# Optimization experiments

Measured on AMD Instinct MI355X. Metric: run time of the kernel, lower is better.

## Reference

```python
import jax, jax.numpy as jnp
import numpy as np

N_VOLS, N_PARTS = 4, 8          # hard-coded in GL.forward
B = N_VOLS * N_PARTS            # asserted batch size = 32
DIM, HID, PROJ = 8192, 4096, 256
TEMP = 0.1
BN_EPS = 1e-5


def setup_inputs() -> dict:
    key = jax.random.key(0)
    k = jax.random.split(key, 5)
    s1 = 1.0 / np.sqrt(DIM)
    s2 = 1.0 / np.sqrt(HID)
    return {
        "x": jax.random.normal(k[0], (B, DIM), jnp.float32),
        "W1": jax.random.uniform(k[1], (DIM, HID), jnp.float32, -s1, s1),
        "b1": jax.random.uniform(k[2], (HID,), jnp.float32, -s1, s1),
        "gamma": jnp.ones((HID,), jnp.float32),
        "beta": jnp.zeros((HID,), jnp.float32),
        "W2": jax.random.uniform(k[3], (HID, PROJ), jnp.float32, -s2, s2),
        "b2": jax.random.uniform(k[4], (PROJ,), jnp.float32, -s2, s2),
    }


def _gl_loss(proj):
    # F.normalize(p=2, dim=-1); CosineSimilarity on unit vectors == dot product
    p = proj / jnp.linalg.norm(proj, axis=-1, keepdims=True)
    sims = (p @ p.T) / TEMP                       # [B, B]
    idx = jnp.arange(B)
    # pos_index(i) = {i % n_parts + v * n_parts} -> same part id; includes i itself
    pos_mask = (idx[:, None] % N_PARTS) == (idx[None, :] % N_PARTS)  # [B, B], 4 per row
    neg_mask = ~pos_mask                                             # 28 per row
    E = jnp.exp(sims)                              # original uses raw exp (no max-shift)
    row_neg = jnp.sum(jnp.where(neg_mask, E, 0.0), axis=1)    # sum_j exp(s[i, neg_j])
    ET = E.T                                        # ET[i, p] = exp(s[p, i])
    col_neg = jnp.sum(jnp.where(neg_mask, ET, 0.0), axis=1)   # sum_j exp(s[neg_j, i])
    t1 = -jnp.log(E / (E + row_neg[:, None]))      # row-direction term per (i, pos)
    t2 = -jnp.log(ET / (ET + col_neg[:, None]))    # column-direction term per (i, pos)
    per_row = jnp.sum(jnp.where(pos_mask, t1 + t2, 0.0), axis=1) / N_VOLS
    return jnp.sum(per_row) / (B * 2)


def reference(x, W1, b1, gamma, beta, W2, b2):
    # projector MLP: Linear -> BatchNorm1d (training stats) -> ReLU -> Linear
    h = x @ W1 + b1
    mu = jnp.mean(h, axis=0)
    var = jnp.var(h, axis=0)                       # biased variance, BN training mode
    h = gamma * (h - mu) * jax.lax.rsqrt(var + BN_EPS) + beta
    h = jax.nn.relu(h)
    proj = h @ W2 + b2                             # [B, PROJ]
    return _gl_loss(proj)
```

## Files before the change

kernel.cpp:

```cpp
#include <hip/hip_runtime.h>

#define DIM   8192
#define HID   4096
#define PROJ  256
#define NB    32
#define KSP1  16
#define KCH1  (DIM / KSP1)
#define KT1   (KCH1 / 32)
#define KSP2  16
#define KCH2  (HID / KSP2)
#define KT2   (KCH2 / 32)

typedef __attribute__((ext_vector_type(8))) short bf16x8;
typedef __attribute__((ext_vector_type(4))) float f32x4;

__device__ __forceinline__ float bf2f(unsigned short u) {
    return __uint_as_float(((unsigned)u) << 16);
}
__device__ __forceinline__ unsigned short f2bf(float f) {
    unsigned u = __float_as_uint(f);
    u += 0x7fffu + ((u >> 16) & 1u);
    return (unsigned short)(u >> 16);
}
__device__ __forceinline__ unsigned pk2(float a, float b) {
    return (unsigned)f2bf(a) | ((unsigned)f2bf(b) << 16);
}

__device__ __forceinline__ bool detect_bf16(const unsigned* __restrict__ xw, int lane) {
    unsigned v = xw[lane];
    int e = (int)((v >> 7) & 0xffu);
    bool pl = (e >= 100 && e <= 135);
    unsigned long long b = __ballot(pl);
    return __popcll(b) >= 32;
}

__global__ __launch_bounds__(256, 4) void gemm1_kernel(
    const void* __restrict__ xv, const void* __restrict__ W1v,
    float* __restrict__ hpart)
{
    const int t  = threadIdx.x;
    const int nb = blockIdx.x & 63;
    const int kc = blockIdx.x >> 6;
    const int k0 = kc * KCH1;

    const bool isbf = detect_bf16((const unsigned*)xv, t & 63);
    const unsigned short* xu  = (const unsigned short*)xv;
    const float*          xf  = (const float*)xv;
    const unsigned short* W1u = (const unsigned short*)W1v;
    const float*          W1f = (const float*)W1v;

    const int lane  = t & 63;
    const int w     = t >> 6;
    const int g     = lane >> 4;
    const int ln    = lane & 15;
    const int nbase = nb * 64 + w * 16;

    auto loadB = [&](int kt) -> bf16x8 {
        bf16x8 b;
        const long rb = (long)(k0 + kt * 32 + g * 8) * HID + nbase + ln;
        if (isbf) {
            #pragma unroll
            for (int j = 0; j < 8; ++j) b[j] = (short)W1u[rb + (long)j * HID];
        } else {
            #pragma unroll
            for (int j = 0; j < 8; ++j) b[j] = (short)f2bf(W1f[rb + (long)j * HID]);
        }
        return b;
    };
    auto loadA = [&](int kt, int mt) -> bf16x8 {
        const int base = (mt * 16 + ln) * DIM + k0 + kt * 32 + g * 8;
        if (isbf) return *(const bf16x8*)(xu + base);
        float4 f0 = *(const float4*)(xf + base);
        float4 f1 = *(const float4*)(xf + base + 4);
        union { uint4 u; bf16x8 v; } c;
        c.u = make_uint4(pk2(f0.x, f0.y), pk2(f0.z, f0.w),
                         pk2(f1.x, f1.y), pk2(f1.z, f1.w));
        return c.v;
    };

    bf16x8 bb[4], a0[4], a1[4];
    #pragma unroll
    for (int i = 0; i < 4; ++i) {
        bb[i] = loadB(i); a0[i] = loadA(i, 0); a1[i] = loadA(i, 1);
    }

    f32x4 acc0 = {0.f, 0.f, 0.f, 0.f};
    f32x4 acc1 = {0.f, 0.f, 0.f, 0.f};

    #pragma unroll
    for (int kt = 0; kt < KT1; ++kt) {
        const int s = kt & 3;
        acc0 = __builtin_amdgcn_mfma_f32_16x16x32_bf16(a0[s], bb[s], acc0, 0, 0, 0);
        acc1 = __builtin_amdgcn_mfma_f32_16x16x32_bf16(a1[s], bb[s], acc1, 0, 0, 0);
        if (kt + 4 < KT1) {
            bb[s] = loadB(kt + 4);
            a0[s] = loadA(kt + 4, 0);
            a1[s] = loadA(kt + 4, 1);
        }
    }

    const int col = nbase + ln;
    #pragma unroll
    for (int r = 0; r < 4; ++r) {
        hpart[(kc * NB + g * 4 + r) * HID + col]      = acc0[r];
        hpart[(kc * NB + 16 + g * 4 + r) * HID + col] = acc1[r];
    }
}

__global__ __launch_bounds__(256) void bnrelu_kernel(
    const float* __restrict__ hpart, const void* __restrict__ gv,
    const void* __restrict__ bev, unsigned short* __restrict__ hrelu,
    const void* __restrict__ xv)
{
    __shared__ float red[16][64];
    __shared__ float ssc[64], sbe[64], smu[64];
    const int t  = threadIdx.x;
    const int c4 = t & 15, q = t >> 4;
    const int n0 = blockIdx.x * 64;
    const int nb = n0 + c4 * 4;
    const bool isbf = detect_bf16((const unsigned*)xv, t & 63);

    f32x4 h0 = {0.f, 0.f, 0.f, 0.f};
    f32x4 h1 = {0.f, 0.f, 0.f, 0.f};
    #pragma unroll
    for (int kc = 0; kc < KSP1; ++kc) {
        h0 += *(const f32x4*)(hpart + (size_t)(kc * 32 + 2 * q) * HID + nb);
        h1 += *(const f32x4*)(hpart + (size_t)(kc * 32 + 2 * q + 1) * HID + nb);
    }
    *(f32x4*)&red[q][c4 * 4] = h0 + h1;
    __syncthreads();
    if (t < 64) {
        float s = 0.f;
        #pragma unroll
        for (int i = 0; i < 16; ++i) s += red[i][t];
        smu[t] = s * (1.f / 32.f);
    }
    __syncthreads();
    const f32x4 mu = *(const f32x4*)&smu[c4 * 4];
    const f32x4 d0 = h0 - mu, d1 = h1 - mu;
    *(f32x4*)&red[q][c4 * 4] = d0 * d0 + d1 * d1;
    __syncthreads();
    if (t < 64) {
        float v = 0.f;
        #pragma unroll
        for (int i = 0; i < 16; ++i) v += red[i][t];
        v *= (1.f / 32.f);
        const int nn = n0 + t;
        const float ga = isbf ? bf2f(((const unsigned short*)gv)[nn])  : ((const float*)gv)[nn];
        const float be = isbf ? bf2f(((const unsigned short*)bev)[nn]) : ((const float*)bev)[nn];
        ssc[t] = ga * rsqrtf(v + 1e-5f);
        sbe[t] = be;
    }
    __syncthreads();
    const f32x4 sc = *(const f32x4*)&ssc[c4 * 4];
    const f32x4 be = *(const f32x4*)&sbe[c4 * 4];
    f32x4 r0 = d0 * sc + be;
    f32x4 r1 = d1 * sc + be;
    ushort4 o0, o1;
    o0.x = f2bf(fmaxf(r0.x, 0.f)); o0.y = f2bf(fmaxf(r0.y, 0.f));
    o0.z = f2bf(fmaxf(r0.z, 0.f)); o0.w = f2bf(fmaxf(r0.w, 0.f));
    o1.x = f2bf(fmaxf(r1.x, 0.f)); o1.y = f2bf(fmaxf(r1.y, 0.f));
    o1.z = f2bf(fmaxf(r1.z, 0.f)); o1.w = f2bf(fmaxf(r1.w, 0.f));
    *(ushort4*)(hrelu + (size_t)(2 * q) * HID + nb)     = o0;
    *(ushort4*)(hrelu + (size_t)(2 * q + 1) * HID + nb) = o1;
}

__global__ __launch_bounds__(256, 4) void gemm2_kernel(
    const unsigned short* __restrict__ hrelu, const void* __restrict__ W2v,
    float* __restrict__ ppart, const void* __restrict__ xv)
{
    const int t  = threadIdx.x;
    const int nb = blockIdx.x & 3;
    const int kc = blockIdx.x >> 2;
    const int k0 = kc * KCH2;

    const bool isbf = detect_bf16((const unsigned*)xv, t & 63);
    const unsigned short* W2u = (const unsigned short*)W2v;
    const float*          W2f = (const float*)W2v;

    const int lane  = t & 63;
    const int w     = t >> 6;
    const int g     = lane >> 4;
    const int ln    = lane & 15;
    const int nbase = nb * 64 + w * 16;

    auto loadB = [&](int kt) -> bf16x8 {
        bf16x8 b;
        const long rb = (long)(k0 + kt * 32 + g * 8) * PROJ + nbase + ln;
        if (isbf) {
            #pragma unroll
            for (int j = 0; j < 8; ++j) b[j] = (short)W2u[rb + (long)j * PROJ];
        } else {
            #pragma unroll
            for (int j = 0; j < 8; ++j) b[j] = (short)f2bf(W2f[rb + (long)j * PROJ]);
        }
        return b;
    };
    auto loadA = [&](int kt, int mt) -> bf16x8 {
        return *(const bf16x8*)(hrelu + (mt * 16 + ln) * HID + k0 + kt * 32 + g * 8);
    };

    bf16x8 bb[4], a0[4], a1[4];
    #pragma unroll
    for (int i = 0; i < 4; ++i) {
        bb[i] = loadB(i); a0[i] = loadA(i, 0); a1[i] = loadA(i, 1);
    }

    f32x4 acc0 = {0.f, 0.f, 0.f, 0.f};
    f32x4 acc1 = {0.f, 0.f, 0.f, 0.f};

    #pragma unroll
    for (int kt = 0; kt < KT2; ++kt) {
        const int s = kt & 3;
        acc0 = __builtin_amdgcn_mfma_f32_16x16x32_bf16(a0[s], bb[s], acc0, 0, 0, 0);
        acc1 = __builtin_amdgcn_mfma_f32_16x16x32_bf16(a1[s], bb[s], acc1, 0, 0, 0);
        if (kt + 4 < KT2) {
            bb[s] = loadB(kt + 4);
            a0[s] = loadA(kt + 4, 0);
            a1[s] = loadA(kt + 4, 1);
        }
    }

    const int col = nbase + ln;
    #pragma unroll
    for (int r = 0; r < 4; ++r) {
        ppart[(kc * NB + g * 4 + r) * PROJ + col]      = acc0[r];
        ppart[(kc * NB + 16 + g * 4 + r) * PROJ + col] = acc1[r];
    }
}

__global__ __launch_bounds__(1024) void loss_kernel(
    const float* __restrict__ ppart, const void* __restrict__ b2v,
    const void* __restrict__ xv, unsigned* __restrict__ out)
{
    __shared__ float ps[32][260];
    __shared__ float npart2[32][8];
    __shared__ float inrm[32];
    __shared__ float rowtot[32];
    const int t = threadIdx.x;
    const bool isbf = detect_bf16((const unsigned*)xv, t & 63);

    #pragma unroll
    for (int i = 0; i < 8; ++i) {
        const int o = i * 1024 + t;
        float s = 0.f;
        #pragma unroll
        for (int s16 = 0; s16 < KSP2; ++s16) s += ppart[s16 * (NB * PROJ) + o];
        const int c = o & 255;
        s += isbf ? bf2f(((const unsigned short*)b2v)[c]) : ((const float*)b2v)[c];
        ps[o >> 8][c] = s;
    }
    __syncthreads();

    if (t < 256) {
        const int r = t >> 3, seg = t & 7;
        float s = 0.f;
        #pragma unroll
        for (int c = 0; c < 32; ++c) { float v = ps[r][seg * 32 + c]; s += v * v; }
        npart2[r][seg] = s;
    }
    __syncthreads();
    if (t < 32) {
        float s = 0.f;
        #pragma unroll
        for (int j = 0; j < 8; ++j) s += npart2[t][j];
        inrm[t] = rsqrtf(s);
    }
    __syncthreads();

    const int wv   = t >> 6;
    const int lane = t & 63;
    const int j    = (lane >> 1) & 31;
    const int half = lane & 1;
    #pragma unroll
    for (int rr = 0; rr < 2; ++rr) {
        const int i = wv * 2 + rr;
        float acc = 0.f;
        const int cb = half * 128;
        #pragma unroll
        for (int c = 0; c < 128; c += 4) {
            float4 a = *(const float4*)&ps[i][cb + c];
            float4 b = *(const float4*)&ps[j][cb + c];
            acc += a.x * b.x + a.y * b.y + a.z * b.z + a.w * b.w;
        }
        acc += __shfl_xor(acc, 1);

        const float sim = acc * inrm[i] * inrm[j] * 10.0f;
        const float E   = __expf(sim);
        const bool pos  = ((j & 7) == (i & 7));

        float nv = (!pos && half == 0) ? E : 0.f;
        #pragma unroll
        for (int s = 1; s < 64; s <<= 1) nv += __shfl_xor(nv, s);
        float pv = (pos && half == 0) ? (logf(E + nv) - sim) : 0.f;
        #pragma unroll
        for (int s = 1; s < 64; s <<= 1) pv += __shfl_xor(pv, s);
        if (lane == 0) rowtot[i] = pv;
    }
    __syncthreads();

    if (t < 64) {
        float v = (t < 32) ? rowtot[t] : 0.f;
        #pragma unroll
        for (int s = 1; s < 64; s <<= 1) v += __shfl_xor(v, s);
        if (t == 0) {
            const float loss = v * (1.0f / 128.0f);
            const unsigned lb = (unsigned)f2bf(loss);
            const unsigned base = (__float_as_uint(loss) & 0xffff0000u) | lb;
            unsigned best = base;
            float ebest = fabsf(__uint_as_float(base) - loss);
            const unsigned cp = base + 0x10000u;
            const float ep = fabsf(__uint_as_float(cp) - loss);
            if (ep < ebest) { best = cp; ebest = ep; }
            const unsigned cm = base - 0x10000u;
            const float em = fabsf(__uint_as_float(cm) - loss);
            if (em < ebest) { best = cm; }
            out[0] = best;
        }
    }
}

extern "C" void kernel_launch(void* const* d_in, const int* in_sizes, int n_in,
                              void* d_out, int out_size, void* d_ws, size_t ws_size,
                              hipStream_t stream) {
    const void* x  = d_in[0];
    const void* W1 = d_in[1];
    const void* ga = d_in[3];
    const void* be = d_in[4];
    const void* W2 = d_in[5];
    const void* b2 = d_in[6];

    char* wsp = (char*)d_ws;
    float* hpart = (float*)wsp;                 wsp += (size_t)KSP1 * NB * HID * 4;
    unsigned short* hrelu = (unsigned short*)wsp; wsp += (size_t)NB * HID * 2;
    float* ppart = (float*)wsp;                 wsp += (size_t)KSP2 * NB * PROJ * 4;

    gemm1_kernel<<<1024, 256, 0, stream>>>(x, W1, hpart);
    bnrelu_kernel<<<64, 256, 0, stream>>>(hpart, ga, be, hrelu, x);
    gemm2_kernel<<<64, 256, 0, stream>>>(hrelu, W2, ppart, x);
    loss_kernel<<<1, 1024, 0, stream>>>(ppart, b2, x, (unsigned*)d_out);
}
```

Baseline: 240.2 us.

## Cut GEMM prefetch depth to two stages and simplify address and pack arithmetic

In both GEMM kernels, the four-deep register prefetch ring is replaced by a two-stage double buffer with explicit A/B slots. Loads are now indexed with precomputed 32-bit base offsets instead of per-load 64-bit address math. The fp32-to-bf16 pack uses a single byte-permute builtin instead of shifts and ors. The aim is fewer VGPRs and less integer overhead, at the cost of fewer loads in flight to hide global-memory latency in a bandwidth-bound GEMM.

```diff
diff --git a/kernel.cpp b/kernel.cpp
--- a/kernel.cpp
+++ b/kernel.cpp
@@ -23,7 +23,11 @@
     return (unsigned short)(u >> 16);
 }
 __device__ __forceinline__ unsigned pk2(float a, float b) {
-    return (unsigned)f2bf(a) | ((unsigned)f2bf(b) << 16);
+    unsigned ua = __float_as_uint(a);
+    unsigned ub = __float_as_uint(b);
+    ua += 0x7fffu + ((ua >> 16) & 1u);
+    ub += 0x7fffu + ((ub >> 16) & 1u);
+    return __builtin_amdgcn_perm(ub, ua, 0x07060302u);
 }
 
 __device__ __forceinline__ bool detect_bf16(const unsigned* __restrict__ xw, int lane) {
@@ -55,20 +59,29 @@
     const int ln    = lane & 15;
     const int nbase = nb * 64 + w * 16;
 
+    const unsigned ubB = (unsigned)(k0 + g * 8) * HID + (unsigned)(nbase + ln);
+    const unsigned ubA0 = (unsigned)(0 * 16 + ln) * DIM + (unsigned)(k0 + g * 8);
+    const unsigned ubA1 = (unsigned)(1 * 16 + ln) * DIM + (unsigned)(k0 + g * 8);
+
     auto loadB = [&](int kt) -> bf16x8 {
-        bf16x8 b;
-        const long rb = (long)(k0 + kt * 32 + g * 8) * HID + nbase + ln;
+        union { unsigned u[4]; bf16x8 v; } r;
         if (isbf) {
             #pragma unroll
-            for (int j = 0; j < 8; ++j) b[j] = (short)W1u[rb + (long)j * HID];
+            for (int j = 0; j < 8; ++j)
+                ((unsigned short*)r.u)[j] = W1u[ubB + (unsigned)(kt * 32 + j) * HID];
         } else {
-            #pragma unroll
-            for (int j = 0; j < 8; ++j) b[j] = (short)f2bf(W1f[rb + (long)j * HID]);
-        }
-        return b;
+            float f[8];
+            #pragma unroll
+            for (int j = 0; j < 8; ++j)
+                f[j] = W1f[ubB + (unsigned)(kt * 32 + j) * HID];
+            #pragma unroll
+            for (int j = 0; j < 4; ++j)
+                r.u[j] = pk2(f[2 * j], f[2 * j + 1]);
+        }
+        return r.v;
     };
     auto loadA = [&](int kt, int mt) -> bf16x8 {
-        const int base = (mt * 16 + ln) * DIM + k0 + kt * 32 + g * 8;
+        const unsigned base = (mt ? ubA1 : ubA0) + (unsigned)(kt * 32);
         if (isbf) return *(const bf16x8*)(xu + base);
         float4 f0 = *(const float4*)(xf + base);
         float4 f1 = *(const float4*)(xf + base + 4);
@@ -78,24 +91,23 @@
         return c.v;
     };
 
-    bf16x8 bb[4], a0[4], a1[4];
-    #pragma unroll
-    for (int i = 0; i < 4; ++i) {
-        bb[i] = loadB(i); a0[i] = loadA(i, 0); a1[i] = loadA(i, 1);
-    }
+    bf16x8 bA  = loadB(0), aA0 = loadA(0, 0), aA1 = loadA(0, 1);
+    bf16x8 bB  = loadB(1), aB0 = loadA(1, 0), aB1 = loadA(1, 1);
 
     f32x4 acc0 = {0.f, 0.f, 0.f, 0.f};
     f32x4 acc1 = {0.f, 0.f, 0.f, 0.f};
 
     #pragma unroll
-    for (int kt = 0; kt < KT1; ++kt) {
-        const int s = kt & 3;
-        acc0 = __builtin_amdgcn_mfma_f32_16x16x32_bf16(a0[s], bb[s], acc0, 0, 0, 0);
-        acc1 = __builtin_amdgcn_mfma_f32_16x16x32_bf16(a1[s], bb[s], acc1, 0, 0, 0);
-        if (kt + 4 < KT1) {
-            bb[s] = loadB(kt + 4);
-            a0[s] = loadA(kt + 4, 0);
-            a1[s] = loadA(kt + 4, 1);
+    for (int kt = 0; kt < KT1; kt += 2) {
+        acc0 = __builtin_amdgcn_mfma_f32_16x16x32_bf16(aA0, bA, acc0, 0, 0, 0);
+        acc1 = __builtin_amdgcn_mfma_f32_16x16x32_bf16(aA1, bA, acc1, 0, 0, 0);
+        if (kt + 2 < KT1) {
+            bA = loadB(kt + 2); aA0 = loadA(kt + 2, 0); aA1 = loadA(kt + 2, 1);
+        }
+        acc0 = __builtin_amdgcn_mfma_f32_16x16x32_bf16(aB0, bB, acc0, 0, 0, 0);
+        acc1 = __builtin_amdgcn_mfma_f32_16x16x32_bf16(aB1, bB, acc1, 0, 0, 0);
+        if (kt + 3 < KT1) {
+            bB = loadB(kt + 3); aB0 = loadA(kt + 3, 0); aB1 = loadA(kt + 3, 1);
         }
     }
 
@@ -184,40 +196,48 @@
     const int ln    = lane & 15;
     const int nbase = nb * 64 + w * 16;
 
+    const unsigned ubB = (unsigned)(k0 + g * 8) * PROJ + (unsigned)(nbase + ln);
+    const unsigned ubA0 = (unsigned)(0 * 16 + ln) * HID + (unsigned)(k0 + g * 8);
+    const unsigned ubA1 = (unsigned)(1 * 16 + ln) * HID + (unsigned)(k0 + g * 8);
+
     auto loadB = [&](int kt) -> bf16x8 {
-        bf16x8 b;
-        const long rb = (long)(k0 + kt * 32 + g * 8) * PROJ + nbase + ln;
+        union { unsigned u[4]; bf16x8 v; } r;
         if (isbf) {
             #pragma unroll
-            for (int j = 0; j < 8; ++j) b[j] = (short)W2u[rb + (long)j * PROJ];
+            for (int j = 0; j < 8; ++j)
+                ((unsigned short*)r.u)[j] = W2u[ubB + (unsigned)(kt * 32 + j) * PROJ];
         } else {
-            #pragma unroll
-            for (int j = 0; j < 8; ++j) b[j] = (short)f2bf(W2f[rb + (long)j * PROJ]);
-        }
-        return b;
+            float f[8];
+            #pragma unroll
+            for (int j = 0; j < 8; ++j)
+                f[j] = W2f[ubB + (unsigned)(kt * 32 + j) * PROJ];
+            #pragma unroll
+            for (int j = 0; j < 4; ++j)
+                r.u[j] = pk2(f[2 * j], f[2 * j + 1]);
+        }
+        return r.v;
     };
     auto loadA = [&](int kt, int mt) -> bf16x8 {
-        return *(const bf16x8*)(hrelu + (mt * 16 + ln) * HID + k0 + kt * 32 + g * 8);
+        return *(const bf16x8*)(hrelu + (mt ? ubA1 : ubA0) + (unsigned)(kt * 32));
     };
 
-    bf16x8 bb[4], a0[4], a1[4];
-    #pragma unroll
-    for (int i = 0; i < 4; ++i) {
-        bb[i] = loadB(i); a0[i] = loadA(i, 0); a1[i] = loadA(i, 1);
-    }
+    bf16x8 bA  = loadB(0), aA0 = loadA(0, 0), aA1 = loadA(0, 1);
+    bf16x8 bB  = loadB(1), aB0 = loadA(1, 0), aB1 = loadA(1, 1);
 
     f32x4 acc0 = {0.f, 0.f, 0.f, 0.f};
     f32x4 acc1 = {0.f, 0.f, 0.f, 0.f};
 
     #pragma unroll
-    for (int kt = 0; kt < KT2; ++kt) {
-        const int s = kt & 3;
-        acc0 = __builtin_amdgcn_mfma_f32_16x16x32_bf16(a0[s], bb[s], acc0, 0, 0, 0);
-        acc1 = __builtin_amdgcn_mfma_f32_16x16x32_bf16(a1[s], bb[s], acc1, 0, 0, 0);
-        if (kt + 4 < KT2) {
-            bb[s] = loadB(kt + 4);
-            a0[s] = loadA(kt + 4, 0);
-            a1[s] = loadA(kt + 4, 1);
+    for (int kt = 0; kt < KT2; kt += 2) {
+        acc0 = __builtin_amdgcn_mfma_f32_16x16x32_bf16(aA0, bA, acc0, 0, 0, 0);
+        acc1 = __builtin_amdgcn_mfma_f32_16x16x32_bf16(aA1, bA, acc1, 0, 0, 0);
+        if (kt + 2 < KT2) {
+            bA = loadB(kt + 2); aA0 = loadA(kt + 2, 0); aA1 = loadA(kt + 2, 1);
+        }
+        acc0 = __builtin_amdgcn_mfma_f32_16x16x32_bf16(aB0, bB, acc0, 0, 0, 0);
+        acc1 = __builtin_amdgcn_mfma_f32_16x16x32_bf16(aB1, bB, acc1, 0, 0, 0);
+        if (kt + 3 < KT2) {
+            bB = loadB(kt + 3); aB0 = loadA(kt + 3, 0); aB1 = loadA(kt + 3, 1);
         }
     }
 
```

Result: no change. 240.3 us (+0.1%).
